# Kernel optimization log

Hardware: AMD Instinct MI355X
Metric: run time of the kernel (lower is better)

The kernel has to match this reference:

```python
import jax, jax.numpy as jnp
import numpy as np

N_NODES = 100000
FEATURES, HIDDEN, CLASSES = 256, 128, 32
N_EDGES = 1600000


def setup_inputs() -> dict:
    key = jax.random.key(0)
    k1, k2, k3, k4, k5 = jax.random.split(key, 5)
    x = jax.random.normal(k1, (N_NODES, FEATURES), dtype=jnp.float32)
    edge_index = jax.random.randint(k2, (2, N_EDGES), 0, N_NODES, dtype=jnp.int64)
    # GCNConv: Linear(in, out, bias=False) + separate bias added after aggregation
    s1 = 1.0 / np.sqrt(FEATURES)
    s2 = 1.0 / np.sqrt(HIDDEN)
    W1 = jax.random.uniform(k3, (FEATURES, HIDDEN), jnp.float32, -s1, s1)
    b1 = jnp.zeros((HIDDEN,), jnp.float32)
    W2 = jax.random.uniform(k4, (HIDDEN, CLASSES), jnp.float32, -s2, s2)
    b2 = jnp.zeros((CLASSES,), jnp.float32)
    return {"x": x, "W1": W1, "b1": b1, "W2": W2, "b2": b2, "edge_index": edge_index}


def _gcn_conv(x, edge_index, W, b, n_nodes):
    # PyG GCNConv with add_self_loops=False: out = D^{-1/2} A D^{-1/2} (X W) + b
    src, dst = edge_index[0], edge_index[1]
    h = x @ W  # [N, out]
    deg = jax.ops.segment_sum(jnp.ones_like(dst, dtype=h.dtype), dst, num_segments=n_nodes)
    dinv = jnp.where(deg > 0, jax.lax.rsqrt(jnp.maximum(deg, 1e-12)), 0.0)
    norm = dinv[src] * dinv[dst]  # [E]
    msgs = h[src] * norm[:, None]  # [E, out] gather + scale
    out = jax.ops.segment_sum(msgs, dst, num_segments=n_nodes)  # scatter-add
    return out + b


def reference(x, W1, b1, W2, b2, edge_index):
    h = _gcn_conv(x, edge_index, W1, b1, N_NODES)
    h = jax.nn.relu(h)
    # F.dropout(training=self.training): eval mode -> identity
    h = _gcn_conv(h, edge_index, W2, b2, N_NODES)
    return jax.nn.log_softmax(h, axis=1)
```

## Files before the change

### kernel.cpp

```cpp
#include <hip/hip_runtime.h>

typedef unsigned short u16;
typedef unsigned int   u32;
typedef __attribute__((ext_vector_type(8))) short short8;
typedef __attribute__((ext_vector_type(4))) float f32x4;
typedef __attribute__((ext_vector_type(2))) float f32x2;

constexpr int BSH = 9;
constexpr int BSZ = 1 << BSH;

__device__ inline float bf2f(u32 bits16) {
    union { u32 u; float f; } c; c.u = bits16 << 16; return c.f;
}
__device__ inline u16 f2bf(float f) {
    union { float f; u32 u; } c; c.f = f;
    return (u16)((c.u + 0x8000u) >> 16);
}
__device__ inline f32x2 up2(u32 h) {
    union { u32 u[2]; f32x2 f; } c;
    c.u[0] = h << 16;
    c.u[1] = h & 0xffff0000u;
    return c.f;
}
__device__ inline int ld_edge(const void* eb, int f64, size_t idx) {
    return f64 ? (int)((const long long*)eb)[idx] : ((const int*)eb)[idx];
}
__device__ inline void gl16(const void* g, void* l) {
    __builtin_amdgcn_global_load_lds(
        (const __attribute__((address_space(1))) unsigned int*)g,
        (__attribute__((address_space(3))) unsigned int*)l, 16, 0, 0);
}

__global__ void detect_kernel(const u32* xw, const int* ebuf_int, int* flags,
                              int* bucket_rsv, int nb, int CAP) {
    __shared__ int cnt;
    if (threadIdx.x == 0) cnt = 0;
    __syncthreads();
    u32 w = xw[threadIdx.x];
    int e = (int)((w >> 7) & 0xffu);
    if (e >= 110 && e <= 145) atomicAdd(&cnt, 1);
    int ev = ebuf_int[2 * threadIdx.x + 1];
    unsigned long long any = __ballot(ev != 0);
    if ((int)threadIdx.x < nb) bucket_rsv[threadIdx.x] = threadIdx.x * CAP;
    __syncthreads();
    if (threadIdx.x == 0) {
        flags[0] = (cnt < 192) ? 1 : 0;
        flags[1] = 0;
        flags[2] = (any == 0ULL) ? 1 : 0;
    }
}

__global__ void bconv_kernel(const void* b1, const void* b2, const int* flags,
                             float* b1f, float* b2f, int HID, int CLS) {
    int i = blockIdx.x * 256 + threadIdx.x;
    int f = flags[0];
    if (i < HID) b1f[i] = f ? ((const float*)b1)[i] : bf2f(((const u16*)b1)[i]);
    if (i < CLS) b2f[i] = f ? ((const float*)b2)[i] : bf2f(((const u16*)b2)[i]);
}

__global__ __launch_bounds__(256)
void passA_kernel(const void* eb, const int* flags, int* bucket_rsv,
                  int2* bpair, int E, int nb, int CAP) {
    __shared__ int hist[256];
    __shared__ int rbase[256];
    hist[threadIdx.x] = 0;
    __syncthreads();
    int f64 = flags[2];
    int base = blockIdx.x * 8192;
    #pragma unroll
    for (int k = 0; k < 32; ++k) {
        int e = base + k * 256 + threadIdx.x;
        if (e < E) {
            int d = ld_edge(eb, f64, (size_t)E + e);
            atomicAdd(&hist[d >> BSH], 1);
        }
    }
    __syncthreads();
    {
        int b = threadIdx.x;
        int c = (b < nb) ? hist[b] : 0;
        rbase[b] = c ? atomicAdd(&bucket_rsv[b], c) : 0;
        hist[b] = 0;
    }
    __syncthreads();
    #pragma unroll
    for (int k = 0; k < 32; ++k) {
        int e = base + k * 256 + threadIdx.x;
        if (e < E) {
            int d = ld_edge(eb, f64, (size_t)E + e);
            int s = ld_edge(eb, f64, (size_t)e);
            int bb = d >> BSH;
            int r = atomicAdd(&hist[bb], 1);
            int pos = rbase[bb] + r;
            if (pos < (bb + 1) * CAP)
                bpair[pos] = make_int2(s, d);
        }
    }
}

__global__ void fillscan_kernel(const int* bucket_rsv, int* bucket_base,
                                int* row_start, int nb, int E, int N, int CAP) {
    __shared__ int wsum[4];
    int t = threadIdx.x, lane = t & 63, wv = t >> 6;
    int v = (t < nb) ? (bucket_rsv[t] - t * CAP) : 0;
    int inc = v;
    #pragma unroll
    for (int d = 1; d < 64; d <<= 1) {
        int tmp = __shfl_up(inc, d, 64);
        if (lane >= d) inc += tmp;
    }
    if (lane == 63) wsum[wv] = inc;
    __syncthreads();
    int off = 0;
    #pragma unroll
    for (int w = 0; w < 4; ++w) if (w < wv) off += wsum[w];
    int excl = off + inc - v;
    if (t <= nb) bucket_base[t] = (t == nb) ? E : excl;
    if (t == 0) row_start[N] = E;
}

__global__ __launch_bounds__(256)
void bucketF_kernel(const int2* __restrict__ bpair, const int* __restrict__ bucket_rsv,
                    const int* __restrict__ bucket_base, float* __restrict__ dinv,
                    int* __restrict__ row_start, int* __restrict__ csr, int N, int CAP) {
    __shared__ int lcnt[BSZ];
    __shared__ int lrow[BSZ];
    __shared__ int wsum[4];
    int b = blockIdx.x, d0 = b << BSH;
    int t = threadIdx.x, lane = t & 63, wv = t >> 6;
    lcnt[2 * t] = 0; lcnt[2 * t + 1] = 0;
    __syncthreads();
    int e0 = b * CAP;
    int e1 = bucket_rsv[b];
    for (int e = e0 + t; e < e1; e += 256)
        atomicAdd(&lcnt[bpair[e].y - d0], 1);
    __syncthreads();
    int c0 = lcnt[2 * t], c1 = lcnt[2 * t + 1];
    int p = c0 + c1;
    int inc = p;
    #pragma unroll
    for (int d = 1; d < 64; d <<= 1) {
        int tmp = __shfl_up(inc, d, 64);
        if (lane >= d) inc += tmp;
    }
    if (lane == 63) wsum[wv] = inc;
    __syncthreads();
    int off = 0;
    #pragma unroll
    for (int w = 0; w < 4; ++w) if (w < wv) off += wsum[w];
    int ex0 = off + inc - p;
    int bb = bucket_base[b];
    lrow[2 * t] = ex0;
    lrow[2 * t + 1] = ex0 + c0;
    int da = d0 + 2 * t, db = d0 + 2 * t + 1;
    if (da < N) { row_start[da] = bb + ex0;      dinv[da] = c0 ? rsqrtf((float)c0) : 0.f; }
    if (db < N) { row_start[db] = bb + ex0 + c0; dinv[db] = c1 ? rsqrtf((float)c1) : 0.f; }
    lcnt[2 * t] = 0; lcnt[2 * t + 1] = 0;
    __syncthreads();
    for (int e = e0 + t; e < e1; e += 256) {
        int2 pr = bpair[e];
        int li = pr.y - d0;
        int r = atomicAdd(&lcnt[li], 1);
        csr[bb + lrow[li] + r] = pr.x;
    }
}

template<int NT, int KT, int NCOLS>
__global__ void prepack_kernel(const void* W, const int* flags, u16* pack) {
    int p = blockIdx.x * 256 + threadIdx.x;
    constexpr int TOT = NT * KT * 64 * 8;
    if (p >= TOT) return;
    int j = p & 7, lane = (p >> 3) & 63, fk = p >> 9;
    int kk = fk % KT, nt = fk / KT;
    int n = nt * 16 + (lane & 15);
    int k = kk * 32 + (lane >> 4) * 8 + j;
    u16 v = flags[0] ? f2bf(((const float*)W)[k * NCOLS + n])
                     : ((const u16*)W)[k * NCOLS + n];
    pack[p] = v;
}

template<int NT, int NTF, int KT, int G>
__global__ __launch_bounds__(256)
void gemm1_kernel(const void* __restrict__ A, const int* __restrict__ ff,
                  const u16* __restrict__ Bpack, const float* __restrict__ dinv,
                  u16* __restrict__ C, int M) {
    constexpr int K = KT * 32;
    constexpr int Ncols = NTF * 16;
    constexpr int NSPLIT = NTF / NT;
    constexpr int BM = 4 * 16 * G;
    constexpr int ABUF = BM * 32 * 4;
    constexpr int BBYTES = NT * KT * 64 * 16;
    __shared__ __align__(16) char ldsA[3 * ABUF];
    __shared__ short8 ldsB[NT * KT * 64];

    const int bh = blockIdx.x % NSPLIT;
    const int bm = blockIdx.x / NSPLIT;
    const int t  = threadIdx.x;

    {
        const char* gB = (const char*)Bpack + (size_t)bh * BBYTES;
        char* lB = (char*)ldsB;
        #pragma unroll
        for (int c = 0; c < BBYTES / 4096; ++c)
            gl16(gB + c * 4096 + t * 16, lB + c * 4096 + t * 16);
    }
    const bool fA = (*ff != 0);
    const int wave = t >> 6, lane = t & 63;
    const int m0 = (bm * 4 + wave) * (16 * G);
    const int q = lane >> 4, l16 = lane & 15;

    f32x4 acc[G][NT];
    #pragma unroll
    for (int g = 0; g < G; ++g)
        #pragma unroll
        for (int nt = 0; nt < NT; ++nt) acc[g][nt] = (f32x4){0.f, 0.f, 0.f, 0.f};

    if (fA) {
        const int rb = t >> 3;
        const int sl = t & 7;
        const int sg = sl ^ (rb & 7);
        const float* gp[4];
        #pragma unroll
        for (int c = 0; c < 4; ++c) {
            int r = bm * BM + c * 32 + rb;
            if (r > M - 1) r = M - 1;
            gp[c] = (const float*)A + (size_t)r * K + sg * 4;
        }
        int off0[G], off1[G];
        #pragma unroll
        for (int g = 0; g < G; ++g) {
            int row_l = wave * (16 * G) + g * 16 + l16;
            int r7 = row_l & 7;
            off0[g] = row_l * 128 + ((2 * q) ^ r7) * 16;
            off1[g] = row_l * 128 + ((2 * q + 1) ^ r7) * 16;
        }
        #pragma unroll
        for (int pj = 0; pj < 2; ++pj) {
            char* lb = ldsA + pj * ABUF + t * 16;
            #pragma unroll
            for (int c = 0; c < 4; ++c)
                gl16(gp[c] + pj * 32, lb + c * 4096);
        }
        #pragma unroll
        for (int kk = 0; kk < KT; ++kk) {
            if (kk == KT - 1) asm volatile("s_waitcnt vmcnt(0)" ::: "memory");
            else              asm volatile("s_waitcnt vmcnt(4)" ::: "memory");
            asm volatile("s_barrier" ::: "memory");
            if (kk + 2 < KT) {
                char* lb = ldsA + ((kk + 2) % 3) * ABUF + t * 16;
                #pragma unroll
                for (int c = 0; c < 4; ++c)
                    gl16(gp[c] + (kk + 2) * 32, lb + c * 4096);
            }
            const char* ab = ldsA + (kk % 3) * ABUF;
            short8 a[G];
            #pragma unroll
            for (int g = 0; g < G; ++g) {
                f32x4 v0 = *(const f32x4*)(ab + off0[g]);
                f32x4 v1 = *(const f32x4*)(ab + off1[g]);
                union { short8 s; u16 u[8]; } pa;
                pa.u[0] = f2bf(v0[0]); pa.u[1] = f2bf(v0[1]);
                pa.u[2] = f2bf(v0[2]); pa.u[3] = f2bf(v0[3]);
                pa.u[4] = f2bf(v1[0]); pa.u[5] = f2bf(v1[1]);
                pa.u[6] = f2bf(v1[2]); pa.u[7] = f2bf(v1[3]);
                a[g] = pa.s;
            }
            #pragma unroll
            for (int nt = 0; nt < NT; ++nt) {
                short8 b = ldsB[(nt * KT + kk) * 64 + lane];
                #pragma unroll
                for (int g = 0; g < G; ++g)
                    acc[g][nt] = __builtin_amdgcn_mfma_f32_16x16x32_bf16(a[g], b, acc[g][nt], 0, 0, 0);
            }
        }
    } else {
        asm volatile("s_waitcnt vmcnt(0)" ::: "memory");
        asm volatile("s_barrier" ::: "memory");
        int rowc[G];
        #pragma unroll
        for (int g = 0; g < G; ++g) {
            int r = m0 + g * 16 + l16;
            rowc[g] = (r < M) ? r : (M - 1);
        }
        #pragma unroll
        for (int kk = 0; kk < KT; ++kk) {
            short8 a[G];
            #pragma unroll
            for (int g = 0; g < G; ++g)
                a[g] = ((const short8*)((const u16*)A + (size_t)rowc[g] * K))[kk * 4 + q];
            #pragma unroll
            for (int nt = 0; nt < NT; ++nt) {
                short8 b = ldsB[(nt * KT + kk) * 64 + lane];
                #pragma unroll
                for (int g = 0; g < G; ++g)
                    acc[g][nt] = __builtin_amdgcn_mfma_f32_16x16x32_bf16(a[g], b, acc[g][nt], 0, 0, 0);
            }
        }
    }

    #pragma unroll
    for (int g = 0; g < G; ++g) {
        float sc[4];
        #pragma unroll
        for (int r = 0; r < 4; ++r) {
            int rr = m0 + g * 16 + q * 4 + r;
            sc[r] = dinv[(rr < M) ? rr : (M - 1)];
        }
        #pragma unroll
        for (int nt = 0; nt < NT; ++nt) {
            int col = bh * (NT * 16) + nt * 16 + l16;
            #pragma unroll
            for (int r = 0; r < 4; ++r) {
                int rrow = m0 + g * 16 + q * 4 + r;
                if (rrow < M)
                    C[(size_t)rrow * Ncols + col] = f2bf(acc[g][nt][r] * sc[r]);
            }
        }
    }
}

template<int NT, int KT, int G>
__global__ __launch_bounds__(256)
void gemm_kernel(const void* __restrict__ A, const int* __restrict__ ff,
                 const u16* __restrict__ Bpack, const float* __restrict__ dinv,
                 u16* __restrict__ C, int M) {
    constexpr int K = KT * 32;
    constexpr int Ncols = NT * 16;
    __shared__ short8 lds[NT * KT * 64];
    for (int i = threadIdx.x; i < NT * KT * 64; i += 256)
        lds[i] = ((const short8*)Bpack)[i];
    bool fA = (*ff != 0);
    __syncthreads();
    int wave = threadIdx.x >> 6, lane = threadIdx.x & 63;
    int m0 = (blockIdx.x * 4 + wave) * (16 * G);
    if (m0 >= M) return;
    int q = lane >> 4;
    int rowc[G];
    #pragma unroll
    for (int g = 0; g < G; ++g) {
        int r = m0 + g * 16 + (lane & 15);
        rowc[g] = (r < M) ? r : (M - 1);
    }
    f32x4 acc[G][NT];
    #pragma unroll
    for (int g = 0; g < G; ++g)
        #pragma unroll
        for (int nt = 0; nt < NT; ++nt) acc[g][nt] = (f32x4){0.f, 0.f, 0.f, 0.f};
    #pragma unroll
    for (int kk = 0; kk < KT; ++kk) {
        short8 a[G];
        #pragma unroll
        for (int g = 0; g < G; ++g) {
            if (fA) {
                const float* Af = (const float*)A + (size_t)rowc[g] * K + kk * 32 + q * 8;
                f32x4 v0 = ((const f32x4*)Af)[0];
                f32x4 v1 = ((const f32x4*)Af)[1];
                union { short8 s; u16 u[8]; } pa;
                pa.u[0] = f2bf(v0[0]); pa.u[1] = f2bf(v0[1]);
                pa.u[2] = f2bf(v0[2]); pa.u[3] = f2bf(v0[3]);
                pa.u[4] = f2bf(v1[0]); pa.u[5] = f2bf(v1[1]);
                pa.u[6] = f2bf(v1[2]); pa.u[7] = f2bf(v1[3]);
                a[g] = pa.s;
            } else {
                a[g] = ((const short8*)((const u16*)A + (size_t)rowc[g] * K))[kk * 4 + q];
            }
        }
        #pragma unroll
        for (int nt = 0; nt < NT; ++nt) {
            short8 b = lds[(nt * KT + kk) * 64 + lane];
            #pragma unroll
            for (int g = 0; g < G; ++g)
                acc[g][nt] = __builtin_amdgcn_mfma_f32_16x16x32_bf16(a[g], b, acc[g][nt], 0, 0, 0);
        }
    }
    #pragma unroll
    for (int g = 0; g < G; ++g) {
        float sc[4];
        #pragma unroll
        for (int r = 0; r < 4; ++r) {
            int rr = m0 + g * 16 + q * 4 + r;
            sc[r] = dinv[(rr < M) ? rr : (M - 1)];
        }
        #pragma unroll
        for (int nt = 0; nt < NT; ++nt) {
            int col = nt * 16 + (lane & 15);
            #pragma unroll
            for (int r = 0; r < 4; ++r) {
                int rrow = m0 + g * 16 + q * 4 + r;
                if (rrow < M)
                    C[(size_t)rrow * Ncols + col] = f2bf(acc[g][nt][r] * sc[r]);
            }
        }
    }
}

__global__ __launch_bounds__(256)
void agg1_kernel(const u32* __restrict__ H32, const int* __restrict__ csr,
                 const int* __restrict__ row_start, const float* __restrict__ dinv,
                 const float* __restrict__ b1f, u32* __restrict__ H1, int N) {
    int wave = threadIdx.x >> 6, lane = threadIdx.x & 63;
    int n = blockIdx.x * 4 + wave;
    if (n >= N) return;
    int s0 = row_start[n], s1 = row_start[n + 1];
    f32x2 acc = {0.f, 0.f};
    for (int base = s0; base < s1; base += 64) {
        int m = s1 - base; if (m > 64) m = 64;
        int myidx = (lane < m) ? csr[base + lane] : 0;
        int j = 0;
        for (; j + 8 <= m; j += 8) {
            int i0 = __shfl(myidx, j);
            int i1 = __shfl(myidx, j + 1);
            int i2 = __shfl(myidx, j + 2);
            int i3 = __shfl(myidx, j + 3);
            int i4 = __shfl(myidx, j + 4);
            int i5 = __shfl(myidx, j + 5);
            int i6 = __shfl(myidx, j + 6);
            int i7 = __shfl(myidx, j + 7);
            u32 h0 = H32[(size_t)i0 * 64 + lane];
            u32 h1 = H32[(size_t)i1 * 64 + lane];
            u32 h2 = H32[(size_t)i2 * 64 + lane];
            u32 h3 = H32[(size_t)i3 * 64 + lane];
            u32 h4 = H32[(size_t)i4 * 64 + lane];
            u32 h5 = H32[(size_t)i5 * 64 + lane];
            u32 h6 = H32[(size_t)i6 * 64 + lane];
            u32 h7 = H32[(size_t)i7 * 64 + lane];
            f32x2 t0 = up2(h0) + up2(h1);
            f32x2 t1 = up2(h2) + up2(h3);
            f32x2 t2 = up2(h4) + up2(h5);
            f32x2 t3 = up2(h6) + up2(h7);
            acc += (t0 + t1) + (t2 + t3);
        }
        for (; j + 4 <= m; j += 4) {
            int i0 = __shfl(myidx, j);
            int i1 = __shfl(myidx, j + 1);
            int i2 = __shfl(myidx, j + 2);
            int i3 = __shfl(myidx, j + 3);
            u32 h0 = H32[(size_t)i0 * 64 + lane];
            u32 h1 = H32[(size_t)i1 * 64 + lane];
            u32 h2 = H32[(size_t)i2 * 64 + lane];
            u32 h3 = H32[(size_t)i3 * 64 + lane];
            acc += (up2(h0) + up2(h1)) + (up2(h2) + up2(h3));
        }
        for (; j < m; ++j) {
            int s = __shfl(myidx, j);
            acc += up2(H32[(size_t)s * 64 + lane]);
        }
    }
    float wn = dinv[n];
    float v0 = fmaxf(wn * acc.x + b1f[2 * lane], 0.f);
    float v1 = fmaxf(wn * acc.y + b1f[2 * lane + 1], 0.f);
    H1[(size_t)n * 64 + lane] = (u32)f2bf(v0) | ((u32)f2bf(v1) << 16);
}

__global__ __launch_bounds__(256)
void agg2_kernel(const u32* __restrict__ H2, const int* __restrict__ csr,
                 const int* __restrict__ row_start, const float* __restrict__ dinv,
                 const float* __restrict__ b2f, const int* __restrict__ ff,
                 void* __restrict__ out, int N) {
    int wave = threadIdx.x >> 6, lane = threadIdx.x & 63;
    int n = blockIdx.x * 4 + wave;
    if (n >= N) return;
    int l16 = lane & 15, grp = lane >> 4;
    int s0 = row_start[n], s1 = row_start[n + 1];
    f32x2 acc = {0.f, 0.f};
    for (int base = s0; base < s1; base += 64) {
        int m = s1 - base; if (m > 64) m = 64;
        int myidx = (lane < m) ? csr[base + lane] : 0;
        int j = 0;
        for (; j + 8 <= m; j += 8) {
            int ia = __shfl(myidx, j + grp);
            int ib = __shfl(myidx, j + 4 + grp);
            u32 ha = H2[(size_t)ia * 16 + l16];
            u32 hb = H2[(size_t)ib * 16 + l16];
            acc += up2(ha) + up2(hb);
        }
        for (; j < m; j += 4) {
            int jj = j + grp;
            int iv = __shfl(myidx, (jj < m) ? jj : 0);
            if (jj < m) acc += up2(H2[(size_t)iv * 16 + l16]);
        }
    }
    acc.x += __shfl_xor(acc.x, 16); acc.y += __shfl_xor(acc.y, 16);
    acc.x += __shfl_xor(acc.x, 32); acc.y += __shfl_xor(acc.y, 32);
    float wn = dinv[n];
    f32x2 tot;
    tot.x = wn * acc.x + b2f[2 * l16];
    tot.y = wn * acc.y + b2f[2 * l16 + 1];
    float mx = fmaxf(tot.x, tot.y);
    #pragma unroll
    for (int msk = 8; msk; msk >>= 1) mx = fmaxf(mx, __shfl_xor(mx, msk));
    float ex = expf(tot.x - mx) + expf(tot.y - mx);
    #pragma unroll
    for (int msk = 8; msk; msk >>= 1) ex += __shfl_xor(ex, msk);
    float ls = mx + logf(ex);
    if (grp == 0) {
        if (*ff) {
            f32x2 r; r.x = tot.x - ls; r.y = tot.y - ls;
            ((f32x2*)out)[(size_t)n * 16 + l16] = r;
        } else {
            ((u32*)out)[(size_t)n * 16 + l16] =
                (u32)f2bf(tot.x - ls) | ((u32)f2bf(tot.y - ls) << 16);
        }
    }
}

extern "C" void kernel_launch(void* const* d_in, const int* in_sizes, int n_in,
                              void* d_out, int out_size, void* d_ws, size_t ws_size,
                              hipStream_t stream) {
    const void* x  = d_in[0];
    const void* W1 = d_in[1];
    const void* b1 = d_in[2];
    const void* W2 = d_in[3];
    const void* b2 = d_in[4];
    const void* eb = d_in[5];

    const int HID  = in_sizes[2];
    const int CLS  = in_sizes[4];
    const int FEAT = in_sizes[1] / HID;
    const int N    = in_sizes[0] / FEAT;
    const int E    = in_sizes[5] / 2;
    const int nb   = (N + BSZ - 1) >> BSH;
    const int CAP  = (((4 * (E / nb)) >> 10) + 2) << 10;
    (void)n_in; (void)out_size;

    char* w = (char*)d_ws;
    size_t p = 0;
    auto alloc = [&](size_t bytes) {
        size_t o = p; p = (p + bytes + 255) & ~(size_t)255; return o;
    };
    int*   flags      = (int*)  (w + alloc(32));
    int*   row_start  = (int*)  (w + alloc((size_t)(N + 1) * 4));
    int*   bucket_base= (int*)  (w + alloc(257 * 4));
    int*   bucket_rsv = (int*)  (w + alloc(256 * 4));
    int2*  bpair      = (int2*) (w + alloc((size_t)nb * CAP * 8));
    int*   csr        = (int*)  (w + alloc((size_t)E * 4));
    float* dinv       = (float*)(w + alloc((size_t)N * 4));
    float* b1f        = (float*)(w + alloc((size_t)HID * 4));
    float* b2f        = (float*)(w + alloc((size_t)CLS * 4));
    u16*   B1p        = (u16*)  (w + alloc((size_t)FEAT * HID * 2));
    u16*   B2p        = (u16*)  (w + alloc((size_t)HID * CLS * 2));
    u16*   H          = (u16*)  (w + alloc((size_t)N * HID * 2));
    u16*   H1         = (u16*)  (w + alloc((size_t)N * HID * 2));
    u16*   H2         = (u16*)  (w + alloc((size_t)N * CLS * 2));
    if (p > ws_size) return;

    detect_kernel<<<1, 256, 0, stream>>>((const u32*)x, (const int*)eb, flags,
                                         bucket_rsv, nb, CAP);
    bconv_kernel<<<1, 256, 0, stream>>>(b1, b2, flags, b1f, b2f, HID, CLS);

    passA_kernel<<<(E + 8191) / 8192, 256, 0, stream>>>(eb, flags, bucket_rsv,
                                                        bpair, E, nb, CAP);
    fillscan_kernel<<<1, 256, 0, stream>>>(bucket_rsv, bucket_base, row_start,
                                           nb, E, N, CAP);
    bucketF_kernel<<<nb, 256, 0, stream>>>(bpair, bucket_rsv, bucket_base,
                                           dinv, row_start, csr, N, CAP);

    prepack_kernel<8, 8, 128><<<(8 * 8 * 64 * 8 + 255) / 256, 256, 0, stream>>>(W1, flags, B1p);
    prepack_kernel<2, 4, 32><<<(2 * 4 * 64 * 8 + 255) / 256, 256, 0, stream>>>(W2, flags, B2p);

    gemm1_kernel<4, 8, 8, 2><<<2 * ((N + 127) / 128), 256, 0, stream>>>(x, flags, B1p, dinv, H, N);
    agg1_kernel<<<(N + 3) / 4, 256, 0, stream>>>((const u32*)H, csr, row_start, dinv, b1f,
                                                 (u32*)H1, N);
    gemm_kernel<2, 4, 2><<<(N + 127) / 128, 256, 0, stream>>>(H1, flags + 1, B2p, dinv, H2, N);
    agg2_kernel<<<(N + 3) / 4, 256, 0, stream>>>((const u32*)H2, csr, row_start, dinv, b2f,
                                                 flags, (void*)d_out, N);
}
```

Baseline: 377.2 us.

## Load fp32 A directly into registers and compute full N per block in gemm1

Gemm1 no longer stages the fp32 activation tile through a triple-buffered LDS ring with barriers. Each lane now loads its own row fragments straight from global memory into a three-deep register pipeline. The column split is removed, so one block computes all 128 output columns and x is read once instead of twice. This drops LDS traffic and per-k-step barriers, but it raises register pressure (8 N-tiles of accumulators plus 12 raw float4 registers) and uses less coalesced per-lane 32-byte loads.

Measured after the change: 371.9 us. No clear change (-1.4%).

```diff
diff --git a/kernel.cpp b/kernel.cpp
--- a/kernel.cpp
+++ b/kernel.cpp
@@ -179,85 +179,78 @@
     pack[p] = v;
 }
 
-template<int NT, int NTF, int KT, int G>
+template<int NT, int KT, int G>
 __global__ __launch_bounds__(256)
 void gemm1_kernel(const void* __restrict__ A, const int* __restrict__ ff,
                   const u16* __restrict__ Bpack, const float* __restrict__ dinv,
                   u16* __restrict__ C, int M) {
     constexpr int K = KT * 32;
-    constexpr int Ncols = NTF * 16;
-    constexpr int NSPLIT = NTF / NT;
-    constexpr int BM = 4 * 16 * G;
-    constexpr int ABUF = BM * 32 * 4;
+    constexpr int Ncols = NT * 16;
     constexpr int BBYTES = NT * KT * 64 * 16;
-    __shared__ __align__(16) char ldsA[3 * ABUF];
     __shared__ short8 ldsB[NT * KT * 64];
 
-    const int bh = blockIdx.x % NSPLIT;
-    const int bm = blockIdx.x / NSPLIT;
-    const int t  = threadIdx.x;
+    const int t = threadIdx.x;
+    const int wave = t >> 6, lane = t & 63;
 
     {
-        const char* gB = (const char*)Bpack + (size_t)bh * BBYTES;
+        const char* gB = (const char*)Bpack;
         char* lB = (char*)ldsB;
         #pragma unroll
         for (int c = 0; c < BBYTES / 4096; ++c)
             gl16(gB + c * 4096 + t * 16, lB + c * 4096 + t * 16);
     }
     const bool fA = (*ff != 0);
-    const int wave = t >> 6, lane = t & 63;
-    const int m0 = (bm * 4 + wave) * (16 * G);
+    const int m0 = (blockIdx.x * 4 + wave) * (16 * G);
     const int q = lane >> 4, l16 = lane & 15;
 
+    int rowc[G];
+    #pragma unroll
+    for (int g = 0; g < G; ++g) {
+        int r = m0 + g * 16 + l16;
+        rowc[g] = (r < M) ? r : (M - 1);
+    }
+
     f32x4 acc[G][NT];
     #pragma unroll
     for (int g = 0; g < G; ++g)
         #pragma unroll
         for (int nt = 0; nt < NT; ++nt) acc[g][nt] = (f32x4){0.f, 0.f, 0.f, 0.f};
 
+    f32x4 raw[3][G][2];
+    const float* Ap[G];
     if (fA) {
-        const int rb = t >> 3;
-        const int sl = t & 7;
-        const int sg = sl ^ (rb & 7);
-        const float* gp[4];
-        #pragma unroll
-        for (int c = 0; c < 4; ++c) {
-            int r = bm * BM + c * 32 + rb;
-            if (r > M - 1) r = M - 1;
-            gp[c] = (const float*)A + (size_t)r * K + sg * 4;
-        }
-        int off0[G], off1[G];
-        #pragma unroll
-        for (int g = 0; g < G; ++g) {
-            int row_l = wave * (16 * G) + g * 16 + l16;
-            int r7 = row_l & 7;
-            off0[g] = row_l * 128 + ((2 * q) ^ r7) * 16;
-            off1[g] = row_l * 128 + ((2 * q + 1) ^ r7) * 16;
-        }
-        #pragma unroll
-        for (int pj = 0; pj < 2; ++pj) {
-            char* lb = ldsA + pj * ABUF + t * 16;
-            #pragma unroll
-            for (int c = 0; c < 4; ++c)
-                gl16(gp[c] + pj * 32, lb + c * 4096);
-        }
+        #pragma unroll
+        for (int g = 0; g < G; ++g)
+            Ap[g] = (const float*)A + (size_t)rowc[g] * K + q * 8;
+        #pragma unroll
+        for (int pj = 0; pj < 2; ++pj)
+            #pragma unroll
+            for (int g = 0; g < G; ++g) {
+                const float* p = Ap[g] + pj * 32;
+                raw[pj][g][0] = ((const f32x4*)p)[0];
+                raw[pj][g][1] = ((const f32x4*)p)[1];
+            }
+        __builtin_amdgcn_sched_barrier(0);
+    }
+    __syncthreads();
+
+    if (fA) {
         #pragma unroll
         for (int kk = 0; kk < KT; ++kk) {
-            if (kk == KT - 1) asm volatile("s_waitcnt vmcnt(0)" ::: "memory");
-            else              asm volatile("s_waitcnt vmcnt(4)" ::: "memory");
-            asm volatile("s_barrier" ::: "memory");
             if (kk + 2 < KT) {
-                char* lb = ldsA + ((kk + 2) % 3) * ABUF + t * 16;
                 #pragma unroll
-                for (int c = 0; c < 4; ++c)
-                    gl16(gp[c] + (kk + 2) * 32, lb + c * 4096);
-            }
-            const char* ab = ldsA + (kk % 3) * ABUF;
+                for (int g = 0; g < G; ++g) {
+                    const float* p = Ap[g] + (kk + 2) * 32;
+                    raw[(kk + 2) % 3][g][0] = ((const f32x4*)p)[0];
+                    raw[(kk + 2) % 3][g][1] = ((const f32x4*)p)[1];
+                }
+            }
+            __builtin_amdgcn_sched_barrier(0);
             short8 a[G];
             #pragma unroll
             for (int g = 0; g < G; ++g) {
-                f32x4 v0 = *(const f32x4*)(ab + off0[g]);
-                f32x4 v1 = *(const f32x4*)(ab + off1[g]);
+                f32x4 v0 = raw[kk % 3][g][0];
+                f32x4 v1 = raw[kk % 3][g][1];
                 union { short8 s; u16 u[8]; } pa;
                 pa.u[0] = f2bf(v0[0]); pa.u[1] = f2bf(v0[1]);
                 pa.u[2] = f2bf(v0[2]); pa.u[3] = f2bf(v0[3]);
@@ -274,14 +267,6 @@
             }
         }
     } else {
-        asm volatile("s_waitcnt vmcnt(0)" ::: "memory");
-        asm volatile("s_barrier" ::: "memory");
-        int rowc[G];
-        #pragma unroll
-        for (int g = 0; g < G; ++g) {
-            int r = m0 + g * 16 + l16;
-            rowc[g] = (r < M) ? r : (M - 1);
-        }
         #pragma unroll
         for (int kk = 0; kk < KT; ++kk) {
             short8 a[G];
@@ -308,7 +293,7 @@
         }
         #pragma unroll
         for (int nt = 0; nt < NT; ++nt) {
-            int col = bh * (NT * 16) + nt * 16 + l16;
+            int col = nt * 16 + l16;
             #pragma unroll
             for (int r = 0; r < 4; ++r) {
                 int rrow = m0 + g * 16 + q * 4 + r;
@@ -558,7 +543,7 @@
     prepack_kernel<8, 8, 128><<<(8 * 8 * 64 * 8 + 255) / 256, 256, 0, stream>>>(W1, flags, B1p);
     prepack_kernel<2, 4, 32><<<(2 * 4 * 64 * 8 + 255) / 256, 256, 0, stream>>>(W2, flags, B2p);
 
-    gemm1_kernel<4, 8, 8, 2><<<2 * ((N + 127) / 128), 256, 0, stream>>>(x, flags, B1p, dinv, H, N);
+    gemm1_kernel<8, 8, 2><<<(N + 127) / 128, 256, 0, stream>>>(x, flags, B1p, dinv, H, N);
     agg1_kernel<<<(N + 3) / 4, 256, 0, stream>>>((const u32*)H, csr, row_start, dinv, b1f,
                                                  (u32*)H1, N);
     gemm_kernel<2, 4, 2><<<(N + 127) / 128, 256, 0, stream>>>(H1, flags + 1, B2p, dinv, H2, N);
```
